# Kernel tuning notes

Hardware: AMD Instinct MI355X
Metric: run time of the kernel (lower is better)

The kernel has to match this reference:

```python
import jax, jax.numpy as jnp
import numpy as np

N, E = 50000, 800000
IN_DIM, HID = 11, 128
EPS = 1e-5

def setup_inputs() -> dict:
    key = jax.random.key(0)
    ks = jax.random.split(key, 20)
    def w(k, i, o):
        return jax.random.normal(k, (i, o), jnp.float32) * (1.0 / np.sqrt(i))
    inp = {}
    inp['x'] = jax.random.normal(ks[0], (N, IN_DIM), jnp.float32)
    inp['edge_index'] = jax.random.randint(ks[1], (2, E), 0, N, jnp.int64)
    dims = [(IN_DIM, HID), (HID, HID), (HID, HID)]
    for i, (di, do) in enumerate(dims):
        inp[f'w_l{i}'] = w(ks[2 + 3 * i], di, do)
        inp[f'b_l{i}'] = jnp.zeros((do,), jnp.float32)
        inp[f'w_r{i}'] = w(ks[3 + 3 * i], di, do)
        inp[f'ln_w{i}'] = jnp.ones((do,), jnp.float32)
        inp[f'ln_b{i}'] = jnp.zeros((do,), jnp.float32)
    inp['c_w0'] = w(ks[12], HID, HID // 2)
    inp['c_b0'] = jnp.zeros((HID // 2,), jnp.float32)
    inp['c_w1'] = w(ks[13], HID // 2, 1)
    inp['c_b1'] = jnp.zeros((1,), jnp.float32)
    return inp

def _sage_conv(x, src, dst, w_l, b_l, w_r):
    # PyG SAGEConv (mean aggr): lin_l(mean_{j in N(i)} x_j) + lin_r(x_i)
    n = x.shape[0]
    agg = jax.ops.segment_sum(x[src], dst, num_segments=n)
    cnt = jax.ops.segment_sum(jnp.ones((src.shape[0], 1), x.dtype), dst, num_segments=n)
    agg = agg / jnp.maximum(cnt, 1.0)
    return agg @ w_l + b_l + x @ w_r

def _layernorm(h, w, b):
    mu = jnp.mean(h, axis=-1, keepdims=True)
    var = jnp.mean(jnp.square(h - mu), axis=-1, keepdims=True)
    return (h - mu) * jax.lax.rsqrt(var + EPS) * w + b

def reference(x, edge_index, w_l0, b_l0, w_r0, ln_w0, ln_b0,
              w_l1, b_l1, w_r1, ln_w1, ln_b1,
              w_l2, b_l2, w_r2, ln_w2, ln_b2,
              c_w0, c_b0, c_w1, c_b1):
    src, dst = edge_index[0], edge_index[1]
    layers = [(w_l0, b_l0, w_r0, ln_w0, ln_b0),
              (w_l1, b_l1, w_r1, ln_w1, ln_b1),
              (w_l2, b_l2, w_r2, ln_w2, ln_b2)]
    for i, (wl, bl, wr, gw, gb) in enumerate(layers):
        h = _sage_conv(x, src, dst, wl, bl, wr)
        h = jax.nn.relu(_layernorm(h, gw, gb))
        # dropout is identity in eval mode
        if i > 0 and h.shape == x.shape:
            h = h + x
        x = h
    h = jax.nn.relu(x @ c_w0 + c_b0)
    out = h @ c_w1 + c_b1
    return out.squeeze(-1)
```

## Files before the change

### kernel.cpp

```cpp
#include <hip/hip_runtime.h>
#include <hip/hip_fp16.h>

#define HID 128

typedef _Float16 h2_t __attribute__((ext_vector_type(2)));

static __device__ __forceinline__ float fdot2(__half2 a, __half2 b, float c) {
    return __builtin_amdgcn_fdot2(__builtin_bit_cast(h2_t, a), __builtin_bit_cast(h2_t, b), c, false);
}

__global__ __launch_bounds__(256) void deg_kernel(const int* __restrict__ ei,
                                                  int* __restrict__ deg, int E, int n) {
    int grp  = blockIdx.x & 7;
    int blk  = blockIdx.x >> 3;
    int nblk = gridDim.x >> 3;
    int lo = (int)(((long long)n * grp) >> 3);
    int hi = (int)(((long long)n * (grp + 1)) >> 3);
    for (int e = blk * 256 + threadIdx.x; e < E; e += nblk * 256) {
        int dst = ei[E + e];
        if (dst >= lo && dst < hi) atomicAdd(&deg[dst], 1);
    }
}

__global__ __launch_bounds__(256) void part_kernel(const int* __restrict__ deg,
                                                   int* __restrict__ part, int n) {
    int i = blockIdx.x * 256 + threadIdx.x;
    int v = (i < n) ? deg[i] : 0;
    #pragma unroll
    for (int m = 1; m < 64; m <<= 1) v += __shfl_xor(v, m);
    __shared__ int w[4];
    int lane = threadIdx.x & 63, wv = threadIdx.x >> 6;
    if (lane == 0) w[wv] = v;
    __syncthreads();
    if (threadIdx.x == 0) part[blockIdx.x] = w[0] + w[1] + w[2] + w[3];
}

__global__ __launch_bounds__(1024) void scanpart_kernel(int* __restrict__ part, int nb) {
    __shared__ int s[1024];
    int t = threadIdx.x;
    int v = (t < nb) ? part[t] : 0;
    int orig = v;
    s[t] = v;
    __syncthreads();
    for (int off = 1; off < 1024; off <<= 1) {
        int u = (t >= off) ? s[t - off] : 0;
        __syncthreads();
        s[t] += u;
        __syncthreads();
    }
    if (t < nb) part[t] = s[t] - orig;
}

__global__ __launch_bounds__(256) void rp_kernel(const int* __restrict__ deg,
                                                 const int* __restrict__ part,
                                                 int* __restrict__ rp,
                                                 int* __restrict__ cursor, int n) {
    int tid = threadIdx.x, lane = tid & 63, wv = tid >> 6;
    int i = blockIdx.x * 256 + tid;
    int v = (i < n) ? deg[i] : 0;
    int orig = v;
    #pragma unroll
    for (int off = 1; off < 64; off <<= 1) {
        int t = __shfl_up(v, off);
        if (lane >= off) v += t;
    }
    __shared__ int wsum[4];
    if (lane == 63) wsum[wv] = v;
    __syncthreads();
    int wbase = 0;
    #pragma unroll
    for (int w = 0; w < 4; ++w) if (w < wv) wbase += wsum[w];
    int excl = part[blockIdx.x] + wbase + v - orig;
    if (i < n) { rp[i] = excl; cursor[i] = excl; }
    if (i == n - 1) rp[n] = excl + orig;
}

__global__ __launch_bounds__(256) void fill_kernel(const int* __restrict__ ei,
                                                   int* __restrict__ cursor,
                                                   int* __restrict__ csr_src, int E, int n) {
    int grp  = blockIdx.x & 7;
    int blk  = blockIdx.x >> 3;
    int nblk = gridDim.x >> 3;
    int lo = (int)(((long long)n * grp) >> 3);
    int hi = (int)(((long long)n * (grp + 1)) >> 3);
    for (int e = blk * 256 + threadIdx.x; e < E; e += nblk * 256) {
        int dst = ei[E + e];
        if (dst >= lo && dst < hi) {
            int pos = atomicAdd(&cursor[dst], 1);
            csr_src[pos] = ei[e];
        }
    }
}

__global__ __launch_bounds__(256) void aggp_kernel(const int* __restrict__ rp,
                                                   const int* __restrict__ ci,
                                                   const __half* __restrict__ h16,
                                                   __half* __restrict__ agg16, int n) {
    int node = (blockIdx.x * 256 + threadIdx.x) >> 6;
    if (node >= n) return;
    int lane = threadIdx.x & 63;
    float2 a0 = make_float2(0.f, 0.f), a1 = make_float2(0.f, 0.f);
    float2 a2 = make_float2(0.f, 0.f), a3 = make_float2(0.f, 0.f);
    float2 a4 = make_float2(0.f, 0.f), a5 = make_float2(0.f, 0.f);
    float2 a6 = make_float2(0.f, 0.f), a7 = make_float2(0.f, 0.f);
    int beg = rp[node], end = rp[node + 1];
    int j = beg;
    for (; j + 7 < end; j += 8) {
        int s0 = ci[j],     s1 = ci[j + 1], s2 = ci[j + 2], s3 = ci[j + 3];
        int s4 = ci[j + 4], s5 = ci[j + 5], s6 = ci[j + 6], s7 = ci[j + 7];
        float2 f0 = __half22float2(*(const __half2*)(h16 + (size_t)s0 * HID + lane * 2));
        float2 f1 = __half22float2(*(const __half2*)(h16 + (size_t)s1 * HID + lane * 2));
        float2 f2 = __half22float2(*(const __half2*)(h16 + (size_t)s2 * HID + lane * 2));
        float2 f3 = __half22float2(*(const __half2*)(h16 + (size_t)s3 * HID + lane * 2));
        float2 f4 = __half22float2(*(const __half2*)(h16 + (size_t)s4 * HID + lane * 2));
        float2 f5 = __half22float2(*(const __half2*)(h16 + (size_t)s5 * HID + lane * 2));
        float2 f6 = __half22float2(*(const __half2*)(h16 + (size_t)s6 * HID + lane * 2));
        float2 f7 = __half22float2(*(const __half2*)(h16 + (size_t)s7 * HID + lane * 2));
        a0.x += f0.x; a0.y += f0.y;  a1.x += f1.x; a1.y += f1.y;
        a2.x += f2.x; a2.y += f2.y;  a3.x += f3.x; a3.y += f3.y;
        a4.x += f4.x; a4.y += f4.y;  a5.x += f5.x; a5.y += f5.y;
        a6.x += f6.x; a6.y += f6.y;  a7.x += f7.x; a7.y += f7.y;
    }
    for (; j + 3 < end; j += 4) {
        int s0 = ci[j], s1 = ci[j + 1], s2 = ci[j + 2], s3 = ci[j + 3];
        float2 f0 = __half22float2(*(const __half2*)(h16 + (size_t)s0 * HID + lane * 2));
        float2 f1 = __half22float2(*(const __half2*)(h16 + (size_t)s1 * HID + lane * 2));
        float2 f2 = __half22float2(*(const __half2*)(h16 + (size_t)s2 * HID + lane * 2));
        float2 f3 = __half22float2(*(const __half2*)(h16 + (size_t)s3 * HID + lane * 2));
        a0.x += f0.x; a0.y += f0.y;  a1.x += f1.x; a1.y += f1.y;
        a2.x += f2.x; a2.y += f2.y;  a3.x += f3.x; a3.y += f3.y;
    }
    for (; j < end; ++j) {
        int s0 = ci[j];
        float2 f0 = __half22float2(*(const __half2*)(h16 + (size_t)s0 * HID + lane * 2));
        a0.x += f0.x; a0.y += f0.y;
    }
    float inv = 1.0f / fmaxf((float)(end - beg), 1.0f);
    float ox = (a0.x + a1.x + a2.x + a3.x + a4.x + a5.x + a6.x + a7.x) * inv;
    float oy = (a0.y + a1.y + a2.y + a3.y + a4.y + a5.y + a6.y + a7.y) * inv;
    *(__half2*)(agg16 + (size_t)node * HID + lane * 2) = __floats2half2_rn(ox, oy);
}

__global__ __launch_bounds__(256) void layer0_kernel(
    const float* __restrict__ x, const int* __restrict__ rp, const int* __restrict__ ci,
    const float* __restrict__ w_l, const float* __restrict__ b_l, const float* __restrict__ w_r,
    const float* __restrict__ ln_w, const float* __restrict__ ln_b,
    __half* __restrict__ h16, int n)
{
    int node = (blockIdx.x * 256 + threadIdx.x) >> 6;
    int lane = threadIdx.x & 63;
    if (node >= n) return;
    int beg = rp[node], end = rp[node + 1];
    int g = lane / 11;
    int d = lane - g * 11;
    float acc0 = 0.f, acc1 = 0.f;
    int j = beg + g;
    if (g < 5) {
        for (; j + 5 < end; j += 10) {
            int s0 = ci[j], s1 = ci[j + 5];
            acc0 += x[(size_t)s0 * 11 + d];
            acc1 += x[(size_t)s1 * 11 + d];
        }
        for (; j < end; j += 5) {
            int s0 = ci[j];
            acc0 += x[(size_t)s0 * 11 + d];
        }
    }
    float acc = acc0 + acc1;
    float aggk = 0.f;
    #pragma unroll
    for (int gg = 0; gg < 5; ++gg) {
        aggk += __shfl(acc, (lane < 11) ? (lane + 11 * gg) : lane);
    }
    float inv = 1.0f / fmaxf((float)(end - beg), 1.0f);
    float v0 = b_l[lane], v1 = b_l[lane + 64];
    #pragma unroll
    for (int k = 0; k < 11; ++k) {
        float a  = __shfl(aggk, k) * inv;
        float xi = x[(size_t)node * 11 + k];
        v0 += a * w_l[k * HID + lane]      + xi * w_r[k * HID + lane];
        v1 += a * w_l[k * HID + lane + 64] + xi * w_r[k * HID + lane + 64];
    }
    float s = v0 + v1, s2 = v0 * v0 + v1 * v1;
    #pragma unroll
    for (int m = 1; m < 64; m <<= 1) { s += __shfl_xor(s, m); s2 += __shfl_xor(s2, m); }
    float mu  = s * (1.0f / HID);
    float var = s2 * (1.0f / HID) - mu * mu;
    float rstd = rsqrtf(var + 1e-5f);
    float o0 = fmaxf((v0 - mu) * rstd * ln_w[lane]      + ln_b[lane],      0.0f);
    float o1 = fmaxf((v1 - mu) * rstd * ln_w[lane + 64] + ln_b[lane + 64], 0.0f);
    h16[(size_t)node * HID + lane]      = __float2half_rn(o0);
    h16[(size_t)node * HID + lane + 64] = __float2half_rn(o1);
}

__global__ __launch_bounds__(256) void wpack_kernel(const float* __restrict__ wl,
                                                    const float* __restrict__ wr,
                                                    __half2* __restrict__ wpk) {
    int idx = blockIdx.x * 256 + threadIdx.x;
    if (idx >= 128 * 128) return;
    int p = idx >> 7, c = idx & 127;
    int k = 2 * p;
    const float* W = (k < HID) ? wl : wr;
    int kk = k & (HID - 1);
    wpk[idx] = __floats2half2_rn(W[kk * HID + c], W[(kk + 1) * HID + c]);
}

__global__ __launch_bounds__(256) void wpack_cls_kernel(const float* __restrict__ w0,
                                                        __half2* __restrict__ w0p) {
    int idx = blockIdx.x * 256 + threadIdx.x;
    if (idx >= 64 * 64) return;
    int p = idx >> 6, c = idx & 63;
    w0p[idx] = __floats2half2_rn(w0[(2 * p) * 64 + c], w0[(2 * p + 1) * 64 + c]);
}

__global__ __launch_bounds__(256) void layer_kernel(
    const __half* __restrict__ agg16, const __half* __restrict__ h16in,
    const __half2* __restrict__ wpk, const float* __restrict__ b_l,
    const float* __restrict__ ln_w, const float* __restrict__ ln_b,
    __half* __restrict__ h16out, int n)
{
    __shared__ __half lds[64][264];
    int base = blockIdx.x * 64;
    int tid = threadIdx.x;
    #pragma unroll
    for (int i = 0; i < 8; ++i) {
        int idx = tid + i * 256;
        int row = idx >> 5;
        int c4  = (idx & 31) * 4;
        int node = base + row;
        float2 a = make_float2(0.f, 0.f);
        float2 h = make_float2(0.f, 0.f);
        if (node < n) {
            a = *(const float2*)(agg16 + (size_t)node * HID + c4);
            h = *(const float2*)(h16in + (size_t)node * HID + c4);
        }
        *(float2*)&lds[row][c4]       = a;
        *(float2*)&lds[row][HID + c4] = h;
    }
    __syncthreads();

    int tx = tid & 31, ty = tid >> 5;
    float acc[8][4];
    #pragma unroll
    for (int r = 0; r < 8; ++r) { acc[r][0] = acc[r][1] = acc[r][2] = acc[r][3] = 0.f; }

    for (int p = 0; p < 128; p += 2) {
        __half2 w00 = wpk[(size_t)(p + 0) * HID + tx * 4 + 0];
        __half2 w01 = wpk[(size_t)(p + 0) * HID + tx * 4 + 1];
        __half2 w02 = wpk[(size_t)(p + 0) * HID + tx * 4 + 2];
        __half2 w03 = wpk[(size_t)(p + 0) * HID + tx * 4 + 3];
        __half2 w10 = wpk[(size_t)(p + 1) * HID + tx * 4 + 0];
        __half2 w11 = wpk[(size_t)(p + 1) * HID + tx * 4 + 1];
        __half2 w12 = wpk[(size_t)(p + 1) * HID + tx * 4 + 2];
        __half2 w13 = wpk[(size_t)(p + 1) * HID + tx * 4 + 3];
        #pragma unroll
        for (int r = 0; r < 8; ++r) {
            float2 raw = *(const float2*)&lds[ty * 8 + r][p * 2];
            const __half2* ap = (const __half2*)&raw;
            __half2 a0 = ap[0], a1 = ap[1];
            acc[r][0] = fdot2(a0, w00, acc[r][0]);
            acc[r][1] = fdot2(a0, w01, acc[r][1]);
            acc[r][2] = fdot2(a0, w02, acc[r][2]);
            acc[r][3] = fdot2(a0, w03, acc[r][3]);
            acc[r][0] = fdot2(a1, w10, acc[r][0]);
            acc[r][1] = fdot2(a1, w11, acc[r][1]);
            acc[r][2] = fdot2(a1, w12, acc[r][2]);
            acc[r][3] = fdot2(a1, w13, acc[r][3]);
        }
    }

    float4 bl = *(const float4*)(b_l  + tx * 4);
    float4 gw = *(const float4*)(ln_w + tx * 4);
    float4 gb = *(const float4*)(ln_b + tx * 4);
    #pragma unroll
    for (int r = 0; r < 8; ++r) {
        float v0 = acc[r][0] + bl.x, v1 = acc[r][1] + bl.y;
        float v2 = acc[r][2] + bl.z, v3 = acc[r][3] + bl.w;
        float s  = v0 + v1 + v2 + v3;
        float s2 = v0*v0 + v1*v1 + v2*v2 + v3*v3;
        #pragma unroll
        for (int m = 16; m >= 1; m >>= 1) { s += __shfl_xor(s, m); s2 += __shfl_xor(s2, m); }
        float mu  = s * (1.0f / HID);
        float var = s2 * (1.0f / HID) - mu * mu;
        float rstd = rsqrtf(var + 1e-5f);
        int row = ty * 8 + r;
        float o0 = fmaxf((v0 - mu) * rstd * gw.x + gb.x, 0.f);
        float o1 = fmaxf((v1 - mu) * rstd * gw.y + gb.y, 0.f);
        float o2 = fmaxf((v2 - mu) * rstd * gw.z + gb.z, 0.f);
        float o3 = fmaxf((v3 - mu) * rstd * gw.w + gb.w, 0.f);
        float2 r01 = __half22float2(*(const __half2*)&lds[row][HID + tx * 4]);
        float2 r23 = __half22float2(*(const __half2*)&lds[row][HID + tx * 4 + 2]);
        o0 += r01.x; o1 += r01.y; o2 += r23.x; o3 += r23.y;
        int node = base + row;
        if (node < n) {
            __half2* d16 = (__half2*)(h16out + (size_t)node * HID + tx * 4);
            d16[0] = __floats2half2_rn(o0, o1);
            d16[1] = __floats2half2_rn(o2, o3);
        }
    }
}

__global__ __launch_bounds__(256) void cls_kernel(
    const __half* __restrict__ h, const __half2* __restrict__ w0p, const float* __restrict__ b0,
    const float* __restrict__ w1, const float* __restrict__ b1, float* __restrict__ out, int n)
{
    __shared__ __half2 w0s[64 * 64];
    int tid = threadIdx.x;
    #pragma unroll
    for (int i = 0; i < 16; ++i) w0s[tid + i * 256] = w0p[tid + i * 256];
    __syncthreads();
    int lane = tid & 63, wv = tid >> 6;
    float bb0 = b0[lane], ww1 = w1[lane], bb1 = b1[0];
    #pragma unroll 1
    for (int q = 0; q < 4; ++q) {
        int node = blockIdx.x * 16 + wv * 4 + q;
        if (node >= n) break;
        const __half2* hr = (const __half2*)(h + (size_t)node * HID);
        float s0 = 0.f, s1 = 0.f;
        #pragma unroll
        for (int p = 0; p < 64; p += 2) {
            s0 = fdot2(hr[p],     w0s[(p + 0) * 64 + lane], s0);
            s1 = fdot2(hr[p + 1], w0s[(p + 1) * 64 + lane], s1);
        }
        float s = fmaxf(s0 + s1 + bb0, 0.f);
        float t = s * ww1;
        #pragma unroll
        for (int m = 1; m < 64; m <<= 1) t += __shfl_xor(t, m);
        if (lane == 0) out[node] = t + bb1;
    }
}

extern "C" void kernel_launch(void* const* d_in, const int* in_sizes, int n_in,
                              void* d_out, int out_size, void* d_ws, size_t ws_size,
                              hipStream_t stream) {
    const float* x  = (const float*)d_in[0];
    const int*   ei = (const int*)d_in[1];
    const float* w_l0 = (const float*)d_in[2];
    const float* b_l0 = (const float*)d_in[3];
    const float* w_r0 = (const float*)d_in[4];
    const float* lnw0 = (const float*)d_in[5];
    const float* lnb0 = (const float*)d_in[6];
    const float* w_l1 = (const float*)d_in[7];
    const float* b_l1 = (const float*)d_in[8];
    const float* w_r1 = (const float*)d_in[9];
    const float* lnw1 = (const float*)d_in[10];
    const float* lnb1 = (const float*)d_in[11];
    const float* w_l2 = (const float*)d_in[12];
    const float* b_l2 = (const float*)d_in[13];
    const float* w_r2 = (const float*)d_in[14];
    const float* lnw2 = (const float*)d_in[15];
    const float* lnb2 = (const float*)d_in[16];
    const float* c_w0 = (const float*)d_in[17];
    const float* c_b0 = (const float*)d_in[18];
    const float* c_w1 = (const float*)d_in[19];
    const float* c_b1 = (const float*)d_in[20];
    float* out = (float*)d_out;

    int N = in_sizes[0] / 11;
    int E = in_sizes[1] / 2;
    int nb = (N + 255) / 256;

    int*     deg    = (int*)d_ws;
    int*     rp     = deg + N;
    int*     cursor = rp + (N + 1);
    int*     csr    = cursor + N;
    int*     part   = csr + E;
    __half*  h16    = (__half*)(part + ((nb + 63) & ~63));
    __half*  agg16  = h16 + (size_t)N * HID;
    __half2* wpk1   = (__half2*)(agg16 + (size_t)N * HID);
    __half2* wpk2   = wpk1 + 128 * HID;
    __half2* w0p    = wpk2 + 128 * HID;

    hipMemsetAsync(deg, 0, (size_t)N * sizeof(int), stream);
    deg_kernel<<<8 * 512, 256, 0, stream>>>(ei, deg, E, N);
    part_kernel<<<nb, 256, 0, stream>>>(deg, part, N);
    scanpart_kernel<<<1, 1024, 0, stream>>>(part, nb);
    rp_kernel<<<nb, 256, 0, stream>>>(deg, part, rp, cursor, N);
    fill_kernel<<<8 * 512, 256, 0, stream>>>(ei, cursor, csr, E, N);
    wpack_kernel<<<64, 256, 0, stream>>>(w_l1, w_r1, wpk1);
    wpack_kernel<<<64, 256, 0, stream>>>(w_l2, w_r2, wpk2);
    wpack_cls_kernel<<<16, 256, 0, stream>>>(c_w0, w0p);

    int nodeBlocks = (N + 3) / 4;

    layer0_kernel<<<nodeBlocks, 256, 0, stream>>>(x, rp, csr, w_l0, b_l0, w_r0, lnw0, lnb0, h16, N);

    aggp_kernel<<<nodeBlocks, 256, 0, stream>>>(rp, csr, h16, agg16, N);
    layer_kernel<<<(N + 63) / 64, 256, 0, stream>>>(agg16, h16, wpk1, b_l1, lnw1, lnb1, h16, N);

    aggp_kernel<<<nodeBlocks, 256, 0, stream>>>(rp, csr, h16, agg16, N);
    layer_kernel<<<(N + 63) / 64, 256, 0, stream>>>(agg16, h16, wpk2, b_l2, lnw2, lnb2, h16, N);

    cls_kernel<<<(N + 15) / 16, 256, 0, stream>>>(h16, w0p, c_b0, c_w1, c_b1, out, N);
}
```

Measured before the change: 324.6 us.

## Use MFMA 16x16x32 f16 instructions for the dense layer GEMM

Replaces the fdot2-based per-thread GEMM in layer_kernel with MFMA 16x16x32 f16 matrix instructions. A new packing kernel lays out the concatenated [W_l; W_r] weights in per-lane MFMA B-fragment order. Each wave computes a 16-row by 128-column tile, and the LayerNorm reduction is remapped to 16-lane shuffles. Output stores become scalar half writes per column tile, which may coalesce less well than the previous half2 stores.

```diff
diff --git a/kernel.cpp b/kernel.cpp
--- a/kernel.cpp
+++ b/kernel.cpp
@@ -4,6 +4,8 @@
 #define HID 128
 
 typedef _Float16 h2_t __attribute__((ext_vector_type(2)));
+typedef _Float16 half8 __attribute__((ext_vector_type(8)));
+typedef float f32x4 __attribute__((ext_vector_type(4)));
 
 static __device__ __forceinline__ float fdot2(__half2 a, __half2 b, float c) {
     return __builtin_amdgcn_fdot2(__builtin_bit_cast(h2_t, a), __builtin_bit_cast(h2_t, b), c, false);
@@ -193,16 +195,23 @@
     h16[(size_t)node * HID + lane + 64] = __float2half_rn(o1);
 }
 
-__global__ __launch_bounds__(256) void wpack_kernel(const float* __restrict__ wl,
+__global__ __launch_bounds__(256) void wfrag_kernel(const float* __restrict__ wl,
                                                     const float* __restrict__ wr,
-                                                    __half2* __restrict__ wpk) {
+                                                    __half* __restrict__ wf) {
     int idx = blockIdx.x * 256 + threadIdx.x;
-    if (idx >= 128 * 128) return;
-    int p = idx >> 7, c = idx & 127;
-    int k = 2 * p;
-    const float* W = (k < HID) ? wl : wr;
-    int kk = k & (HID - 1);
-    wpk[idx] = __floats2half2_rn(W[kk * HID + c], W[(kk + 1) * HID + c]);
+    if (idx >= 4096) return;
+    int kt = idx >> 9;
+    int ct = (idx >> 6) & 7;
+    int l  = idx & 63;
+    int col = ct * 16 + (l & 15);
+    int kbase = kt * 32 + (l >> 4) * 8;
+    #pragma unroll
+    for (int j = 0; j < 8; ++j) {
+        int k = kbase + j;
+        const float* W = (k < HID) ? wl : wr;
+        int kk = k & (HID - 1);
+        wf[(size_t)idx * 8 + j] = __float2half_rn(W[kk * HID + col]);
+    }
 }
 
 __global__ __launch_bounds__(256) void wpack_cls_kernel(const float* __restrict__ w0,
@@ -215,7 +224,7 @@
 
 __global__ __launch_bounds__(256) void layer_kernel(
     const __half* __restrict__ agg16, const __half* __restrict__ h16in,
-    const __half2* __restrict__ wpk, const float* __restrict__ b_l,
+    const __half* __restrict__ wf, const float* __restrict__ b_l,
     const float* __restrict__ ln_w, const float* __restrict__ ln_b,
     __half* __restrict__ h16out, int n)
 {
@@ -239,63 +248,55 @@
     }
     __syncthreads();
 
-    int tx = tid & 31, ty = tid >> 5;
-    float acc[8][4];
-    #pragma unroll
-    for (int r = 0; r < 8; ++r) { acc[r][0] = acc[r][1] = acc[r][2] = acc[r][3] = 0.f; }
-
-    for (int p = 0; p < 128; p += 2) {
-        __half2 w00 = wpk[(size_t)(p + 0) * HID + tx * 4 + 0];
-        __half2 w01 = wpk[(size_t)(p + 0) * HID + tx * 4 + 1];
-        __half2 w02 = wpk[(size_t)(p + 0) * HID + tx * 4 + 2];
-        __half2 w03 = wpk[(size_t)(p + 0) * HID + tx * 4 + 3];
-        __half2 w10 = wpk[(size_t)(p + 1) * HID + tx * 4 + 0];
-        __half2 w11 = wpk[(size_t)(p + 1) * HID + tx * 4 + 1];
-        __half2 w12 = wpk[(size_t)(p + 1) * HID + tx * 4 + 2];
-        __half2 w13 = wpk[(size_t)(p + 1) * HID + tx * 4 + 3];
-        #pragma unroll
-        for (int r = 0; r < 8; ++r) {
-            float2 raw = *(const float2*)&lds[ty * 8 + r][p * 2];
-            const __half2* ap = (const __half2*)&raw;
-            __half2 a0 = ap[0], a1 = ap[1];
-            acc[r][0] = fdot2(a0, w00, acc[r][0]);
-            acc[r][1] = fdot2(a0, w01, acc[r][1]);
-            acc[r][2] = fdot2(a0, w02, acc[r][2]);
-            acc[r][3] = fdot2(a0, w03, acc[r][3]);
-            acc[r][0] = fdot2(a1, w10, acc[r][0]);
-            acc[r][1] = fdot2(a1, w11, acc[r][1]);
-            acc[r][2] = fdot2(a1, w12, acc[r][2]);
-            acc[r][3] = fdot2(a1, w13, acc[r][3]);
-        }
-    }
-
-    float4 bl = *(const float4*)(b_l  + tx * 4);
-    float4 gw = *(const float4*)(ln_w + tx * 4);
-    float4 gb = *(const float4*)(ln_b + tx * 4);
-    #pragma unroll
-    for (int r = 0; r < 8; ++r) {
-        float v0 = acc[r][0] + bl.x, v1 = acc[r][1] + bl.y;
-        float v2 = acc[r][2] + bl.z, v3 = acc[r][3] + bl.w;
-        float s  = v0 + v1 + v2 + v3;
-        float s2 = v0*v0 + v1*v1 + v2*v2 + v3*v3;
-        #pragma unroll
-        for (int m = 16; m >= 1; m >>= 1) { s += __shfl_xor(s, m); s2 += __shfl_xor(s2, m); }
+    int w = tid >> 6;
+    int l = tid & 63;
+    int g = l >> 4, cl = l & 15;
+
+    f32x4 acc[8];
+    #pragma unroll
+    for (int ct = 0; ct < 8; ++ct) acc[ct] = (f32x4){0.f, 0.f, 0.f, 0.f};
+
+    #pragma unroll
+    for (int kt = 0; kt < 8; ++kt) {
+        half8 a = *(const half8*)&lds[w * 16 + cl][kt * 32 + g * 8];
+        #pragma unroll
+        for (int ct = 0; ct < 8; ++ct) {
+            half8 b = *(const half8*)(wf + ((size_t)(kt * 8 + ct) * 64 + l) * 8);
+            acc[ct] = __builtin_amdgcn_mfma_f32_16x16x32_f16(a, b, acc[ct], 0, 0, 0);
+        }
+    }
+
+    float bl8[8], gw8[8], gb8[8];
+    #pragma unroll
+    for (int ct = 0; ct < 8; ++ct) {
+        bl8[ct] = b_l[ct * 16 + cl];
+        gw8[ct] = ln_w[ct * 16 + cl];
+        gb8[ct] = ln_b[ct * 16 + cl];
+    }
+
+    #pragma unroll
+    for (int r = 0; r < 4; ++r) {
+        int row = w * 16 + g * 4 + r;
+        float v[8];
+        float s = 0.f, s2 = 0.f;
+        #pragma unroll
+        for (int ct = 0; ct < 8; ++ct) {
+            v[ct] = acc[ct][r] + bl8[ct];
+            s += v[ct]; s2 += v[ct] * v[ct];
+        }
+        #pragma unroll
+        for (int m = 1; m < 16; m <<= 1) { s += __shfl_xor(s, m); s2 += __shfl_xor(s2, m); }
         float mu  = s * (1.0f / HID);
         float var = s2 * (1.0f / HID) - mu * mu;
         float rstd = rsqrtf(var + 1e-5f);
-        int row = ty * 8 + r;
-        float o0 = fmaxf((v0 - mu) * rstd * gw.x + gb.x, 0.f);
-        float o1 = fmaxf((v1 - mu) * rstd * gw.y + gb.y, 0.f);
-        float o2 = fmaxf((v2 - mu) * rstd * gw.z + gb.z, 0.f);
-        float o3 = fmaxf((v3 - mu) * rstd * gw.w + gb.w, 0.f);
-        float2 r01 = __half22float2(*(const __half2*)&lds[row][HID + tx * 4]);
-        float2 r23 = __half22float2(*(const __half2*)&lds[row][HID + tx * 4 + 2]);
-        o0 += r01.x; o1 += r01.y; o2 += r23.x; o3 += r23.y;
         int node = base + row;
         if (node < n) {
-            __half2* d16 = (__half2*)(h16out + (size_t)node * HID + tx * 4);
-            d16[0] = __floats2half2_rn(o0, o1);
-            d16[1] = __floats2half2_rn(o2, o3);
+            #pragma unroll
+            for (int ct = 0; ct < 8; ++ct) {
+                float o = fmaxf((v[ct] - mu) * rstd * gw8[ct] + gb8[ct], 0.f)
+                          + __half2float(lds[row][HID + ct * 16 + cl]);
+                h16out[(size_t)node * HID + ct * 16 + cl] = __float2half_rn(o);
+            }
         }
     }
 }
@@ -367,9 +368,9 @@
     int*     part   = csr + E;
     __half*  h16    = (__half*)(part + ((nb + 63) & ~63));
     __half*  agg16  = h16 + (size_t)N * HID;
-    __half2* wpk1   = (__half2*)(agg16 + (size_t)N * HID);
-    __half2* wpk2   = wpk1 + 128 * HID;
-    __half2* w0p    = wpk2 + 128 * HID;
+    __half*  wf1    = agg16 + (size_t)N * HID;
+    __half*  wf2    = wf1 + 4096 * 8;
+    __half2* w0p    = (__half2*)(wf2 + 4096 * 8);
 
     hipMemsetAsync(deg, 0, (size_t)N * sizeof(int), stream);
     deg_kernel<<<8 * 512, 256, 0, stream>>>(ei, deg, E, N);
@@ -377,8 +378,8 @@
     scanpart_kernel<<<1, 1024, 0, stream>>>(part, nb);
     rp_kernel<<<nb, 256, 0, stream>>>(deg, part, rp, cursor, N);
     fill_kernel<<<8 * 512, 256, 0, stream>>>(ei, cursor, csr, E, N);
-    wpack_kernel<<<64, 256, 0, stream>>>(w_l1, w_r1, wpk1);
-    wpack_kernel<<<64, 256, 0, stream>>>(w_l2, w_r2, wpk2);
+    wfrag_kernel<<<16, 256, 0, stream>>>(w_l1, w_r1, wf1);
+    wfrag_kernel<<<16, 256, 0, stream>>>(w_l2, w_r2, wf2);
     wpack_cls_kernel<<<16, 256, 0, stream>>>(c_w0, w0p);
 
     int nodeBlocks = (N + 3) / 4;
@@ -386,10 +387,10 @@
     layer0_kernel<<<nodeBlocks, 256, 0, stream>>>(x, rp, csr, w_l0, b_l0, w_r0, lnw0, lnb0, h16, N);
 
     aggp_kernel<<<nodeBlocks, 256, 0, stream>>>(rp, csr, h16, agg16, N);
-    layer_kernel<<<(N + 63) / 64, 256, 0, stream>>>(agg16, h16, wpk1, b_l1, lnw1, lnb1, h16, N);
+    layer_kernel<<<(N + 63) / 64, 256, 0, stream>>>(agg16, h16, wf1, b_l1, lnw1, lnb1, h16, N);
 
     aggp_kernel<<<nodeBlocks, 256, 0, stream>>>(rp, csr, h16, agg16, N);
-    layer_kernel<<<(N + 63) / 64, 256, 0, stream>>>(agg16, h16, wpk2, b_l2, lnw2, lnb2, h16, N);
+    layer_kernel<<<(N + 63) / 64, 256, 0, stream>>>(agg16, h16, wf2, b_l2, lnw2, lnb2, h16, N);
 
     cls_kernel<<<(N + 15) / 16, 256, 0, stream>>>(h16, w0p, c_b0, c_w1, c_b1, out, N);
 }
```

Result: faster. 269.3 us (-17.0%).
